# Optimization experiments

Measured on AMD Instinct MI355X. Metric: run time of the kernel, lower is better.

## Reference

```python
import jax, jax.numpy as jnp
import numpy as np

N = 50000       # nodes
E = 800000      # edges
C_IN = 64
C_OUT = 64
G = 128         # graphs in the batch
EPS = 1e-5      # BatchNorm eps


def setup_inputs() -> dict:
    key = jax.random.key(0)
    ks = jax.random.split(key, 9)
    x = jax.random.normal(ks[0], (N, C_IN), jnp.float32)
    edge_index = jax.random.randint(ks[1], (2, E), 0, N, dtype=jnp.int32)
    edge_weight = jax.random.uniform(ks[2], (E,), jnp.float32)
    batch = jnp.sort(jax.random.randint(ks[3], (N,), 0, G, dtype=jnp.int32))
    # SGConv linear params
    W = jax.random.normal(ks[4], (C_OUT, C_IN), jnp.float32) / np.sqrt(C_IN)
    b = 0.01 * jax.random.normal(ks[5], (C_OUT,), jnp.float32)
    # PReLU per-channel slope (torch init 0.25; perturb to exercise math)
    a = 0.25 + 0.01 * jax.random.normal(ks[6], (C_OUT,), jnp.float32)
    # BatchNorm affine params
    gamma = 1.0 + 0.1 * jax.random.normal(ks[7], (C_OUT,), jnp.float32)
    beta = 0.1 * jax.random.normal(ks[8], (C_OUT,), jnp.float32)
    return {"x": x, "edge_index": edge_index, "edge_weight": edge_weight,
            "batch": batch, "W": W, "b": b, "a": a, "gamma": gamma, "beta": beta}


def reference(x, edge_index, edge_weight, batch, W, b, a, gamma, beta):
    n = x.shape[0]
    loop = jnp.arange(n)
    # gcn_norm with self-loops (SGConv default)
    row = jnp.concatenate([edge_index[0], loop])      # source
    col = jnp.concatenate([edge_index[1], loop])      # target
    w = jnp.concatenate([edge_weight, jnp.ones((n,), x.dtype)])
    deg = jax.ops.segment_sum(w, col, num_segments=n)
    dinv = jnp.where(deg > 0, jax.lax.rsqrt(jnp.where(deg > 0, deg, 1.0)), 0.0)
    norm = dinv[row] * w * dinv[col]
    # K=2 hops of A_hat @ h, then linear
    h = x
    for _ in range(2):
        h = jax.ops.segment_sum(norm[:, None] * h[row], col, num_segments=n)
    h = h @ W.T + b
    # PReLU (per-channel)
    h = jnp.where(h >= 0, h, a * h)
    # BatchNorm1d, training-mode forward (batch stats, biased var)
    mu = h.mean(axis=0)
    var = jnp.mean((h - mu) ** 2, axis=0)
    h = (h - mu) * jax.lax.rsqrt(var + EPS) * gamma + beta
    # Global mean + max pooling per graph -> [G, 2*C_OUT]
    cnt = jax.ops.segment_sum(jnp.ones((n,), h.dtype), batch, num_segments=G)
    mean_p = jax.ops.segment_sum(h, batch, num_segments=G) / jnp.maximum(cnt, 1.0)[:, None]
    max_p = jax.ops.segment_max(h, batch, num_segments=G)
    return jnp.concatenate([mean_p, max_p], axis=1)
```

## Files before the change

### kernel.cpp

```cpp
#include <hip/hip_runtime.h>
#include <hip/hip_bf16.h>
#include <math.h>

#define NN 50000
#define NE 800000
#define CC 64
#define GG 128
#define BINS ((NN + 255) / 256)
#define CAPB 4608
#define EPB 2048
#define GA ((NE + EPB - 1) / EPB)

typedef __hip_bfloat16 bf16;

__device__ inline unsigned short f2b(float f) {
    bf16 h = __float2bfloat16(f);
    return *reinterpret_cast<unsigned short*>(&h);
}
__device__ inline float blo(unsigned u) { return __uint_as_float(u << 16); }
__device__ inline float bhi(unsigned u) { return __uint_as_float(u & 0xffff0000u); }

__global__ void k_prep(int* bin_cnt, float* stats) {
    int t = threadIdx.x;
    if (t < BINS) bin_cnt[t] = 0;
    if (t < 2 * CC) stats[t] = 0.0f;
}

__global__ __launch_bounds__(256) void k_binA(const int* __restrict__ ei,
                                              const float* __restrict__ w,
                                              int* __restrict__ bin_cnt,
                                              int2* __restrict__ binbuf) {
    __shared__ int hist[BINS], base[BINS], rank[BINS];
    __shared__ int cstg[EPB];
    int t = threadIdx.x;
    for (int b = t; b < BINS; b += 256) { hist[b] = 0; rank[b] = 0; }
    __syncthreads();
    int e0 = blockIdx.x * EPB;
    for (int i = t; i < EPB; i += 256) {
        int e = e0 + i;
        if (e < NE) {
            int c = ei[NE + e];
            cstg[i] = c;
            atomicAdd(&hist[c >> 8], 1);
        }
    }
    __syncthreads();
    for (int b = t; b < BINS; b += 256)
        if (hist[b] > 0) base[b] = atomicAdd(&bin_cnt[b], hist[b]);
    __syncthreads();
    for (int i = t; i < EPB; i += 256) {
        int e = e0 + i;
        if (e >= NE) continue;
        int r = ei[e], c = cstg[i], b = c >> 8;
        int pos = base[b] + atomicAdd(&rank[b], 1);
        if (pos < CAPB)
            binbuf[(size_t)b * CAPB + pos] = make_int2(r | ((c & 255) << 16),
                                                       __float_as_int(w[e]));
    }
}

__global__ __launch_bounds__(256) void k_csr(const int* __restrict__ bin_cnt,
                                             int2* __restrict__ binbuf,
                                             float* __restrict__ dinv,
                                             int* __restrict__ rps,
                                             int* __restrict__ rcnt) {
    __shared__ int2 ed[CAPB];
    __shared__ int hist[256], off[256], rank[256];
    __shared__ float degf[256];
    int g = blockIdx.x, t = threadIdx.x;
    int cnt = min(bin_cnt[g], CAPB);
    int2* bp = binbuf + (size_t)g * CAPB;
    hist[t] = 0; rank[t] = 0; degf[t] = 1.0f;
    __syncthreads();
    for (int e = t; e < cnt; e += 256) {
        int2 r = bp[e];
        ed[e] = r;
        int low = r.x >> 16;
        atomicAdd(&hist[low], 1);
        atomicAdd(&degf[low], __int_as_float(r.y));
    }
    __syncthreads();
    int v = hist[t];
    off[t] = v;
    __syncthreads();
    for (int o = 1; o < 256; o <<= 1) {
        int x = (t >= o) ? off[t - o] : 0;
        __syncthreads();
        off[t] += x;
        __syncthreads();
    }
    int node = g * 256 + t;
    if (node < NN) {
        dinv[node] = rsqrtf(degf[t]);
        rps[node] = g * CAPB + (off[t] - v);
        rcnt[node] = v;
    }
    for (int e = t; e < cnt; e += 256) {
        int2 r = ed[e];
        int low = r.x >> 16;
        int pos = (off[low] - hist[low]) + atomicAdd(&rank[low], 1);
        bp[pos] = make_int2(r.x & 0xffff, r.y);
    }
}

__global__ __launch_bounds__(256) void k_linfold(const float* __restrict__ x,
                                                 const float* __restrict__ W,
                                                 const float* __restrict__ dinv,
                                                 const int* __restrict__ rps,
                                                 const int* __restrict__ rcnt,
                                                 const int2* __restrict__ binbuf,
                                                 unsigned* __restrict__ csrc,
                                                 bf16* __restrict__ y) {
    __shared__ float Ws[CC * 65];
    __shared__ float hs[4][CC];
    int tid = threadIdx.x, wv = tid >> 6, j = tid & 63;
    for (int t = tid; t < CC * CC; t += 256)
        Ws[(t >> 6) * 65 + (t & 63)] = W[t];
    int node = blockIdx.x * 4 + wv;
    hs[wv][j] = (node < NN) ? x[node * CC + j] : 0.0f;
    __syncthreads();
    if (node >= NN) return;
    float acc = 0.0f;
    const float* hr = hs[wv];
#pragma unroll
    for (int k = 0; k < CC; k++) acc += hr[k] * Ws[j * 65 + k];
    y[node * CC + j] = __float2bfloat16(acc);
    float dn = dinv[node];
    int s = rps[node], n = rcnt[node];
    for (int p = j; p < n; p += 64) {
        int2 rec = binbuf[s + p];
        float nw = dinv[rec.x] * __int_as_float(rec.y) * dn;
        csrc[s + p] = (unsigned)rec.x | ((unsigned)f2b(nw) << 16);
    }
}

__global__ __launch_bounds__(256) void k_hop8(const bf16* __restrict__ in,
                                              const float* __restrict__ dinv,
                                              const int* __restrict__ rps,
                                              const int* __restrict__ rcnt,
                                              const unsigned* __restrict__ csrc,
                                              bf16* __restrict__ out) {
    int node = blockIdx.x * 4 + (threadIdx.x >> 6);
    if (node >= NN) return;
    int lane = threadIdx.x & 63;
    int o = lane >> 3;
    int lc = lane & 7;
    float dn = dinv[node];
    float a0 = 0, a1 = 0, a2 = 0, a3 = 0, a4 = 0, a5 = 0, a6 = 0, a7 = 0;
    if (o == 0) {
        uint4 v = *reinterpret_cast<const uint4*>(&in[node * CC + 8 * lc]);
        float d2 = dn * dn;
        a0 = d2 * blo(v.x); a1 = d2 * bhi(v.x);
        a2 = d2 * blo(v.y); a3 = d2 * bhi(v.y);
        a4 = d2 * blo(v.z); a5 = d2 * bhi(v.z);
        a6 = d2 * blo(v.w); a7 = d2 * bhi(v.w);
    }
    int s = rps[node], n = rcnt[node];
    const unsigned* cp = csrc + s;
    int p = 0;
#pragma unroll 2
    for (; p + 8 <= n; p += 8) {
        unsigned rec = cp[p + o];
        float nw = bhi(rec);
        int src = rec & 0xffff;
        uint4 v = *reinterpret_cast<const uint4*>(&in[src * CC + 8 * lc]);
        a0 = fmaf(nw, blo(v.x), a0); a1 = fmaf(nw, bhi(v.x), a1);
        a2 = fmaf(nw, blo(v.y), a2); a3 = fmaf(nw, bhi(v.y), a3);
        a4 = fmaf(nw, blo(v.z), a4); a5 = fmaf(nw, bhi(v.z), a5);
        a6 = fmaf(nw, blo(v.w), a6); a7 = fmaf(nw, bhi(v.w), a7);
    }
    if (p < n && o < n - p) {
        unsigned rec = cp[p + o];
        float nw = bhi(rec);
        int src = rec & 0xffff;
        uint4 v = *reinterpret_cast<const uint4*>(&in[src * CC + 8 * lc]);
        a0 = fmaf(nw, blo(v.x), a0); a1 = fmaf(nw, bhi(v.x), a1);
        a2 = fmaf(nw, blo(v.y), a2); a3 = fmaf(nw, bhi(v.y), a3);
        a4 = fmaf(nw, blo(v.z), a4); a5 = fmaf(nw, bhi(v.z), a5);
        a6 = fmaf(nw, blo(v.w), a6); a7 = fmaf(nw, bhi(v.w), a7);
    }
#pragma unroll
    for (int d = 8; d < 64; d <<= 1) {
        a0 += __shfl_xor(a0, d, 64); a1 += __shfl_xor(a1, d, 64);
        a2 += __shfl_xor(a2, d, 64); a3 += __shfl_xor(a3, d, 64);
        a4 += __shfl_xor(a4, d, 64); a5 += __shfl_xor(a5, d, 64);
        a6 += __shfl_xor(a6, d, 64); a7 += __shfl_xor(a7, d, 64);
    }
    if (o == 0) {
        uint4 ov;
        ov.x = (unsigned)f2b(a0) | ((unsigned)f2b(a1) << 16);
        ov.y = (unsigned)f2b(a2) | ((unsigned)f2b(a3) << 16);
        ov.z = (unsigned)f2b(a4) | ((unsigned)f2b(a5) << 16);
        ov.w = (unsigned)f2b(a6) | ((unsigned)f2b(a7) << 16);
        *reinterpret_cast<uint4*>(&out[node * CC + 8 * lc]) = ov;
    }
}

__device__ inline int lbound(const int* __restrict__ batch, int g) {
    int lo = 0, hi = NN;
    while (lo < hi) {
        int mid = (lo + hi) >> 1;
        if (batch[mid] < g) lo = mid + 1; else hi = mid;
    }
    return lo;
}

__global__ __launch_bounds__(256) void k_poolstat(const bf16* __restrict__ h,
                                                  const float* __restrict__ bvec,
                                                  const float* __restrict__ a,
                                                  const int* __restrict__ batch,
                                                  float* __restrict__ stats,
                                                  float* __restrict__ gsum,
                                                  float* __restrict__ gmax,
                                                  float* __restrict__ gmin,
                                                  int* __restrict__ gcnt) {
    __shared__ float r0[4][CC], r1[4][CC], r2[4][CC];
    __shared__ int sse[2];
    int g = blockIdx.x;
    int tid = threadIdx.x, w = tid >> 6, j = tid & 63;
    if (tid == 0) sse[0] = lbound(batch, g);
    if (tid == 1) sse[1] = lbound(batch, g + 1);
    __syncthreads();
    int s = sse[0], e = sse[1];
    float bs = bvec[j], as = a[j];
    float sum = 0.0f, sq = 0.0f, mx = -__builtin_inff(), mn = __builtin_inff();
    for (int i = s + w; i < e; i += 4) {
        float v = __bfloat162float(h[i * CC + j]) + bs;
        v = v >= 0.0f ? v : as * v;
        sum += v;
        sq += v * v;
        mx = fmaxf(mx, v);
        mn = fminf(mn, v);
    }
    r0[w][j] = sum; r1[w][j] = mx; r2[w][j] = mn;
    __syncthreads();
    if (w == 0) {
        sum = r0[0][j] + r0[1][j] + r0[2][j] + r0[3][j];
        mx = fmaxf(fmaxf(r1[0][j], r1[1][j]), fmaxf(r1[2][j], r1[3][j]));
        mn = fminf(fminf(r2[0][j], r2[1][j]), fminf(r2[2][j], r2[3][j]));
        gsum[g * CC + j] = sum;
        gmax[g * CC + j] = mx;
        gmin[g * CC + j] = mn;
        if (j == 0) gcnt[g] = e - s;
        atomicAdd(&stats[j], sum);
    }
    __syncthreads();
    r0[w][j] = sq;
    __syncthreads();
    if (w == 0) {
        sq = r0[0][j] + r0[1][j] + r0[2][j] + r0[3][j];
        atomicAdd(&stats[CC + j], sq);
    }
}

__global__ void k_finish(const float* __restrict__ stats,
                         const float* __restrict__ gamma,
                         const float* __restrict__ beta,
                         const int* __restrict__ gcnt,
                         const float* __restrict__ gsum,
                         const float* __restrict__ gmax,
                         const float* __restrict__ gmin,
                         float* __restrict__ out) {
    int t = blockIdx.x * 256 + threadIdx.x;
    if (t >= GG * CC) return;
    int g = t >> 6, j = t & 63;
    float mean = stats[j] * (1.0f / NN);
    float var = stats[CC + j] * (1.0f / NN) - mean * mean;
    float sc = gamma[j] * rsqrtf(var + 1e-5f);
    float sh = beta[j] - mean * sc;
    int n = gcnt[g];
    if (n > 0) {
        out[g * 2 * CC + j] = sc * (gsum[t] / (float)n) + sh;
        out[g * 2 * CC + CC + j] = (sc >= 0.0f) ? sc * gmax[t] + sh
                                                : sc * gmin[t] + sh;
    } else {
        out[g * 2 * CC + j] = 0.0f;
        out[g * 2 * CC + CC + j] = -__builtin_inff();
    }
}

extern "C" void kernel_launch(void* const* d_in, const int* in_sizes, int n_in,
                              void* d_out, int out_size, void* d_ws, size_t ws_size,
                              hipStream_t stream) {
    const float* x = (const float*)d_in[0];
    const int* ei = (const int*)d_in[1];
    const float* ew = (const float*)d_in[2];
    const int* batch = (const int*)d_in[3];
    const float* W = (const float*)d_in[4];
    const float* b = (const float*)d_in[5];
    const float* a = (const float*)d_in[6];
    const float* gamma = (const float*)d_in[7];
    const float* beta = (const float*)d_in[8];
    float* out = (float*)d_out;

    float* ws = (float*)d_ws;
    float* dinv = ws;
    int* rps = (int*)(ws + 50048);
    int* rcnt = (int*)(ws + 2 * 50048);
    int* bin_cnt = (int*)(ws + 3 * 50048);
    float* stats = ws + 3 * 50048 + 256;
    int* gcnt = (int*)(stats + 256);
    float* gsum = (float*)(gcnt + 256);
    float* gmax = gsum + GG * CC;
    float* gmin = gmax + GG * CC;
    int2* binbuf = (int2*)(gmin + GG * CC);
    unsigned* csrc = (unsigned*)(binbuf + (size_t)BINS * CAPB);
    bf16* y = (bf16*)(csrc + (size_t)BINS * CAPB);
    bf16* h1 = y + (size_t)NN * CC;
    bf16* h2 = h1 + (size_t)NN * CC;

    dim3 blk(256);
    int gH = (NN + 3) / 4;

    k_prep<<<1, blk, 0, stream>>>(bin_cnt, stats);
    k_binA<<<GA, blk, 0, stream>>>(ei, ew, bin_cnt, binbuf);
    k_csr<<<BINS, blk, 0, stream>>>(bin_cnt, binbuf, dinv, rps, rcnt);
    k_linfold<<<gH, blk, 0, stream>>>(x, W, dinv, rps, rcnt, binbuf, csrc, y);

    k_hop8<<<gH, blk, 0, stream>>>(y, dinv, rps, rcnt, csrc, h1);
    k_hop8<<<gH, blk, 0, stream>>>(h1, dinv, rps, rcnt, csrc, h2);

    k_poolstat<<<GG, blk, 0, stream>>>(h2, b, a, batch, stats, gsum, gmax, gmin, gcnt);
    k_finish<<<(GG * CC + 255) / 256, blk, 0, stream>>>(stats, gamma, beta, gcnt,
                                                        gsum, gmax, gmin, out);
}
```

Baseline: 153.9 us.

## Split features into two channel-half planes and run each hop per half

The feature matrices are now stored as two planar halves of 32 channels each instead of 64-wide rows. Each hop runs as two launches, one per half, so each pass gathers from a 3.2MB table that fits cache better. Within a pass, 4 lanes cover a row and 16 edges are processed at a time. The cost is re-reading the CSR edge list twice per hop, extra launches, and a strided access pattern in pooling.

Result: slower. 195.1 us (+26.8%).

```diff
diff --git a/kernel.cpp b/kernel.cpp
--- a/kernel.cpp
+++ b/kernel.cpp
@@ -10,6 +10,7 @@
 #define CAPB 4608
 #define EPB 2048
 #define GA ((NE + EPB - 1) / EPB)
+#define PL (NN * 32)
 
 typedef __hip_bfloat16 bf16;
 
@@ -124,7 +125,7 @@
     const float* hr = hs[wv];
 #pragma unroll
     for (int k = 0; k < CC; k++) acc += hr[k] * Ws[j * 65 + k];
-    y[node * CC + j] = __float2bfloat16(acc);
+    y[(j >> 5) * PL + node * 32 + (j & 31)] = __float2bfloat16(acc);
     float dn = dinv[node];
     int s = rps[node], n = rcnt[node];
     for (int p = j; p < n; p += 64) {
@@ -134,7 +135,7 @@
     }
 }
 
-__global__ __launch_bounds__(256) void k_hop8(const bf16* __restrict__ in,
+__global__ __launch_bounds__(256) void k_hopc(const bf16* __restrict__ in,
                                               const float* __restrict__ dinv,
                                               const int* __restrict__ rps,
                                               const int* __restrict__ rcnt,
@@ -143,12 +144,12 @@
     int node = blockIdx.x * 4 + (threadIdx.x >> 6);
     if (node >= NN) return;
     int lane = threadIdx.x & 63;
-    int o = lane >> 3;
-    int lc = lane & 7;
+    int grp = lane >> 2;
+    int lc = lane & 3;
     float dn = dinv[node];
     float a0 = 0, a1 = 0, a2 = 0, a3 = 0, a4 = 0, a5 = 0, a6 = 0, a7 = 0;
-    if (o == 0) {
-        uint4 v = *reinterpret_cast<const uint4*>(&in[node * CC + 8 * lc]);
+    if (grp == 0) {
+        uint4 v = *reinterpret_cast<const uint4*>(&in[node * 32 + 8 * lc]);
         float d2 = dn * dn;
         a0 = d2 * blo(v.x); a1 = d2 * bhi(v.x);
         a2 = d2 * blo(v.y); a3 = d2 * bhi(v.y);
@@ -158,41 +159,40 @@
     int s = rps[node], n = rcnt[node];
     const unsigned* cp = csrc + s;
     int p = 0;
-#pragma unroll 2
-    for (; p + 8 <= n; p += 8) {
-        unsigned rec = cp[p + o];
+    for (; p + 16 <= n; p += 16) {
+        unsigned rec = cp[p + grp];
         float nw = bhi(rec);
         int src = rec & 0xffff;
-        uint4 v = *reinterpret_cast<const uint4*>(&in[src * CC + 8 * lc]);
+        uint4 v = *reinterpret_cast<const uint4*>(&in[src * 32 + 8 * lc]);
         a0 = fmaf(nw, blo(v.x), a0); a1 = fmaf(nw, bhi(v.x), a1);
         a2 = fmaf(nw, blo(v.y), a2); a3 = fmaf(nw, bhi(v.y), a3);
         a4 = fmaf(nw, blo(v.z), a4); a5 = fmaf(nw, bhi(v.z), a5);
         a6 = fmaf(nw, blo(v.w), a6); a7 = fmaf(nw, bhi(v.w), a7);
     }
-    if (p < n && o < n - p) {
-        unsigned rec = cp[p + o];
+    if (p < n && grp < n - p) {
+        unsigned rec = cp[p + grp];
         float nw = bhi(rec);
         int src = rec & 0xffff;
-        uint4 v = *reinterpret_cast<const uint4*>(&in[src * CC + 8 * lc]);
+        uint4 v = *reinterpret_cast<const uint4*>(&in[src * 32 + 8 * lc]);
         a0 = fmaf(nw, blo(v.x), a0); a1 = fmaf(nw, bhi(v.x), a1);
         a2 = fmaf(nw, blo(v.y), a2); a3 = fmaf(nw, bhi(v.y), a3);
         a4 = fmaf(nw, blo(v.z), a4); a5 = fmaf(nw, bhi(v.z), a5);
         a6 = fmaf(nw, blo(v.w), a6); a7 = fmaf(nw, bhi(v.w), a7);
     }
 #pragma unroll
-    for (int d = 8; d < 64; d <<= 1) {
+    for (int d = 4; d < 64; d <<= 1) {
         a0 += __shfl_xor(a0, d, 64); a1 += __shfl_xor(a1, d, 64);
         a2 += __shfl_xor(a2, d, 64); a3 += __shfl_xor(a3, d, 64);
         a4 += __shfl_xor(a4, d, 64); a5 += __shfl_xor(a5, d, 64);
         a6 += __shfl_xor(a6, d, 64); a7 += __shfl_xor(a7, d, 64);
     }
-    if (o == 0) {
+    if (grp == 0) {
         uint4 ov;
         ov.x = (unsigned)f2b(a0) | ((unsigned)f2b(a1) << 16);
         ov.y = (unsigned)f2b(a2) | ((unsigned)f2b(a3) << 16);
         ov.z = (unsigned)f2b(a4) | ((unsigned)f2b(a5) << 16);
         ov.w = (unsigned)f2b(a6) | ((unsigned)f2b(a7) << 16);
-        *reinterpret_cast<uint4*>(&out[node * CC + 8 * lc]) = ov;
+        *reinterpret_cast<uint4*>(&out[node * 32 + 8 * lc]) = ov;
     }
 }
 
@@ -222,10 +222,11 @@
     if (tid == 1) sse[1] = lbound(batch, g + 1);
     __syncthreads();
     int s = sse[0], e = sse[1];
+    const bf16* hp = h + (j >> 5) * PL + (j & 31);
     float bs = bvec[j], as = a[j];
     float sum = 0.0f, sq = 0.0f, mx = -__builtin_inff(), mn = __builtin_inff();
     for (int i = s + w; i < e; i += 4) {
-        float v = __bfloat162float(h[i * CC + j]) + bs;
+        float v = __bfloat162float(hp[i * 32]) + bs;
         v = v >= 0.0f ? v : as * v;
         sum += v;
         sq += v * v;
@@ -317,8 +318,10 @@
     k_csr<<<BINS, blk, 0, stream>>>(bin_cnt, binbuf, dinv, rps, rcnt);
     k_linfold<<<gH, blk, 0, stream>>>(x, W, dinv, rps, rcnt, binbuf, csrc, y);
 
-    k_hop8<<<gH, blk, 0, stream>>>(y, dinv, rps, rcnt, csrc, h1);
-    k_hop8<<<gH, blk, 0, stream>>>(h1, dinv, rps, rcnt, csrc, h2);
+    k_hopc<<<gH, blk, 0, stream>>>(y,        dinv, rps, rcnt, csrc, h1);
+    k_hopc<<<gH, blk, 0, stream>>>(y + PL,   dinv, rps, rcnt, csrc, h1 + PL);
+    k_hopc<<<gH, blk, 0, stream>>>(h1,       dinv, rps, rcnt, csrc, h2);
+    k_hopc<<<gH, blk, 0, stream>>>(h1 + PL,  dinv, rps, rcnt, csrc, h2 + PL);
 
     k_poolstat<<<GG, blk, 0, stream>>>(h2, b, a, batch, stats, gsum, gmax, gmin, gcnt);
     k_finish<<<(GG * CC + 255) / 256, blk, 0, stream>>>(stats, gamma, beta, gcnt,
```
